# Kernel optimization log

Measured on AMD Instinct MI355X. Metric: run time of the kernel, lower is better.

## Reference

```python
import jax, jax.numpy as jnp
import numpy as np

N_NODES = 50000
D = 128
DROP_P = 0.2


def sage_conv(x, edge_index, W_l, W_r, b):
    # PyG SAGEConv (mean aggr): out = lin_l(mean_j x_j) + lin_r(x)
    src, dst = edge_index[0], edge_index[1]
    n = x.shape[0]
    agg = jax.ops.segment_sum(x[src], dst, num_segments=n)          # [N, F]
    cnt = jax.ops.segment_sum(jnp.ones((src.shape[0],), x.dtype), dst, num_segments=n)
    mean = agg / jnp.maximum(cnt, 1.0)[:, None]
    return mean @ W_l.T + x @ W_r.T + b


def setup_inputs() -> dict:
    key = jax.random.key(0)
    ks = jax.random.split(key, 9)
    x = jax.random.normal(ks[0], (N_NODES, D), dtype=jnp.float32)
    edge_index = jax.random.randint(ks[1], (2, 800000), 0, N_NODES, dtype=jnp.int64)
    s = 1.0 / np.sqrt(D)
    W1_l = jax.random.uniform(ks[2], (D, D), jnp.float32, -s, s)
    W1_r = jax.random.uniform(ks[3], (D, D), jnp.float32, -s, s)
    b1 = jax.random.uniform(ks[4], (D,), jnp.float32, -s, s)
    W2_l = jax.random.uniform(ks[5], (D, D), jnp.float32, -s, s)
    W2_r = jax.random.uniform(ks[6], (D, D), jnp.float32, -s, s)
    b2 = jax.random.uniform(ks[7], (D,), jnp.float32, -s, s)
    return {"x": x, "edge_index": edge_index, "W1_l": W1_l, "W1_r": W1_r,
            "b1": b1, "W2_l": W2_l, "W2_r": W2_r, "b2": b2}


def reference(x, edge_index, W1_l, W1_r, b1, W2_l, W2_r, b2):
    h = sage_conv(x, edge_index, W1_l, W1_r, b1)
    h = jax.nn.relu(h)
    # F.dropout(p=0.2) defaults to training=True; deterministic fixed-key mask
    keep = jax.random.bernoulli(jax.random.key(42), 1.0 - DROP_P, h.shape)
    h = jnp.where(keep, h / (1.0 - DROP_P), 0.0)
    return sage_conv(h, edge_index, W2_l, W2_r, b2)
```

## Files before the change

kernel.cpp:

```cpp
#include <hip/hip_runtime.h>
#include <stdint.h>

#define N_NODES 50000
#define D 128
#define N_EDGES 800000
#define NBUCK 196
#define BCAP 8192
#define EPB 4096

typedef __attribute__((ext_vector_type(8))) short bf16x8;
typedef __attribute__((ext_vector_type(4))) float f32x4;

__device__ __forceinline__ unsigned short f2bf(float f){
  unsigned u = __float_as_uint(f);
  u = u + 0x7FFFu + ((u >> 16) & 1u);
  return (unsigned short)(u >> 16);
}
__device__ __forceinline__ void acc2(float& a, float& b, unsigned w){
  a += __uint_as_float(w << 16);
  b += __uint_as_float(w & 0xFFFF0000u);
}

__device__ __forceinline__ unsigned rotl32(unsigned x, int r){
  return (x << r) | (x >> (32 - r));
}
__device__ __forceinline__ float dropout_factor(unsigned idx){
  unsigned x0 = 0u, x1 = idx;
  const unsigned ks0 = 0u;
  const unsigned ks1 = 42u;
  const unsigned ks2 = 0x1BD11BDAu ^ 0u ^ 42u;
  x0 += ks0; x1 += ks1;
  #define TFR(r) { x0 += x1; x1 = rotl32(x1,(r)); x1 ^= x0; }
  TFR(13) TFR(15) TFR(26) TFR(6)   x0 += ks1; x1 += ks2 + 1u;
  TFR(17) TFR(29) TFR(16) TFR(24)  x0 += ks2; x1 += ks0 + 2u;
  TFR(13) TFR(15) TFR(26) TFR(6)   x0 += ks0; x1 += ks1 + 3u;
  TFR(17) TFR(29) TFR(16) TFR(24)  x0 += ks1; x1 += ks2 + 4u;
  TFR(13) TFR(15) TFR(26) TFR(6)   x0 += ks2; x1 += ks0 + 5u;
  #undef TFR
  unsigned bits = x0 ^ x1;
  float u = __uint_as_float(0x3F800000u | (bits >> 9)) - 1.0f;
  return (u < 0.8f) ? 1.25f : 0.0f;
}

__global__ __launch_bounds__(256) void prep_kernel(
    const float* __restrict__ x,
    const float* __restrict__ W1l, const float* __restrict__ W1r,
    const float* __restrict__ W2l, const float* __restrict__ W2r,
    unsigned short* __restrict__ A1cat,
    unsigned short* __restrict__ Wcat1, unsigned short* __restrict__ Wcat2,
    int* __restrict__ gcursor, const void* __restrict__ ei, int* __restrict__ flag)
{
  int b = blockIdx.x, t = threadIdx.x;
  if (b < 6250){
    int i = b * 256 + t;
    int r = i >> 5, c4 = (i & 31) * 4;
    float4 v = *(const float4*)(x + (size_t)r * 128 + c4);
    ushort4 o = make_ushort4(f2bf(v.x), f2bf(v.y), f2bf(v.z), f2bf(v.w));
    *(ushort4*)(A1cat + (size_t)r * 256 + 128 + c4) = o;
  } else if (b < 6506){
    int c = (b < 6378) ? (b - 6250) : (b - 6378);
    const float* Wl = (b < 6378) ? W1l : W2l;
    const float* Wr = (b < 6378) ? W1r : W2r;
    unsigned short* Wc = (b < 6378) ? Wcat1 : Wcat2;
    float v = (t < 128) ? Wl[c * 128 + t] : Wr[c * 128 + (t - 128)];
    Wc[c * 256 + t] = f2bf(v);
  } else if (b == 6506){
    if (t < NBUCK) gcursor[t] = 0;
  } else {
    __shared__ int nz;
    if (t == 0) nz = 0;
    __syncthreads();
    const int* p = (const int*)ei;
    int local = 0;
    for (int i = t; i < 1024; i += 256)
      if (p[2 * i + 1] != 0) local = 1;
    if (local) atomicAdd(&nz, 1);
    __syncthreads();
    if (t == 0) *flag = (nz == 0) ? 1 : 0;
  }
}

__global__ __launch_bounds__(256) void bucket_kernel(const void* __restrict__ ei,
                                                     const int* __restrict__ flag,
                                                     int* __restrict__ gcursor,
                                                     int* __restrict__ buck){
  __shared__ int hist[NBUCK];
  __shared__ int baseoff[NBUCK];
  const int t = threadIdx.x;
  const int base = blockIdx.x * EPB;
  for (int i = t; i < NBUCK; i += 256) hist[i] = 0;
  __syncthreads();

  int pk[16], bk[16], rk[16];
  #pragma unroll
  for (int j = 0; j < 16; ++j) bk[j] = -1;

  if (*flag){
    const long long* p = (const long long*)ei;
    #pragma unroll
    for (int k = 0; k < 8; ++k){
      int e = base + (k * 256 + t) * 2;
      if (e < N_EDGES){
        int4 vs = *(const int4*)(p + e);
        int4 vd = *(const int4*)(p + N_EDGES + e);
        int ss0 = vs.x, ss1 = vs.z, dd0 = vd.x, dd1 = vd.z;
        int j0 = k * 2, j1 = k * 2 + 1;
        bk[j0] = dd0 >> 8; pk[j0] = (ss0 << 8) | (dd0 & 255);
        rk[j0] = atomicAdd(&hist[bk[j0]], 1);
        bk[j1] = dd1 >> 8; pk[j1] = (ss1 << 8) | (dd1 & 255);
        rk[j1] = atomicAdd(&hist[bk[j1]], 1);
      }
    }
  } else {
    const int* p = (const int*)ei;
    #pragma unroll
    for (int k = 0; k < 4; ++k){
      int e = base + (k * 256 + t) * 4;
      if (e < N_EDGES){
        int4 vs = *(const int4*)(p + e);
        int4 vd = *(const int4*)(p + N_EDGES + e);
        int ss[4] = {vs.x, vs.y, vs.z, vs.w};
        int dd[4] = {vd.x, vd.y, vd.z, vd.w};
        #pragma unroll
        for (int j = 0; j < 4; ++j){
          int slot = k * 4 + j;
          int d = dd[j];
          bk[slot] = d >> 8;
          pk[slot] = (ss[j] << 8) | (d & 255);
          rk[slot] = atomicAdd(&hist[bk[slot]], 1);
        }
      }
    }
  }
  __syncthreads();
  for (int i = t; i < NBUCK; i += 256){
    int h = hist[i];
    baseoff[i] = h ? atomicAdd(&gcursor[i], h) : 0;
  }
  __syncthreads();
  #pragma unroll
  for (int j = 0; j < 16; ++j){
    if (bk[j] >= 0)
      buck[bk[j] * BCAP + baseoff[bk[j]] + rk[j]] = pk[j];
  }
}

__global__ __launch_bounds__(256) void bscan_kernel(const int* __restrict__ gcursor,
                                                    int* __restrict__ bucket_base,
                                                    int* __restrict__ rowptr){
  __shared__ int s[256];
  int t = threadIdx.x;
  s[t] = (t < NBUCK) ? gcursor[t] : 0;
  __syncthreads();
  #pragma unroll
  for (int off = 1; off < 256; off <<= 1){
    int u = (t >= off) ? s[t - off] : 0;
    __syncthreads();
    s[t] += u;
    __syncthreads();
  }
  if (t < NBUCK) bucket_base[t] = (t == 0) ? 0 : s[t - 1];
  if (t == 0){ bucket_base[NBUCK] = N_EDGES; rowptr[N_NODES] = N_EDGES; }
}

__global__ __launch_bounds__(256) void csr_kernel(const int* __restrict__ gcursor,
                                                  const int* __restrict__ bucket_base,
                                                  const int* __restrict__ buck,
                                                  unsigned short* __restrict__ csr16,
                                                  int* __restrict__ rowptr){
  __shared__ int h[256];
  __shared__ int s[256];
  __shared__ int cur[256];
  const int b = blockIdx.x, t = threadIdx.x;
  const int cntb  = gcursor[b];
  const int gbase = bucket_base[b];
  h[t] = 0;
  __syncthreads();
  for (int i = t; i < cntb; i += 256)
    atomicAdd(&h[buck[b * BCAP + i] & 255], 1);
  __syncthreads();
  s[t] = h[t];
  __syncthreads();
  #pragma unroll
  for (int off = 1; off < 256; off <<= 1){
    int u = (t >= off) ? s[t - off] : 0;
    __syncthreads();
    s[t] += u;
    __syncthreads();
  }
  int excl = s[t] - h[t];
  int node = b * 256 + t;
  if (node < N_NODES) rowptr[node] = gbase + excl;
  cur[t] = gbase + excl;
  __syncthreads();
  for (int i = t; i < cntb; i += 256){
    int pkv = buck[b * BCAP + i];
    int pos = atomicAdd(&cur[pkv & 255], 1);
    csr16[pos] = (unsigned short)(((unsigned)pkv) >> 8);
  }
}

__global__ __launch_bounds__(256) void agg_bf16_kernel(
    unsigned short* __restrict__ Acat, const int* __restrict__ rowptr,
    const unsigned short* __restrict__ csr16)
{
  int node = blockIdx.x * 4 + (threadIdx.x >> 6);
  int lane = threadIdx.x & 63;
  if (node >= N_NODES) return;
  int q  = lane >> 4;
  int fl = lane & 15;
  int e0 = rowptr[node], e1 = rowptr[node + 1];
  float s0=0.f,s1=0.f,s2=0.f,s3=0.f,s4=0.f,s5=0.f,s6=0.f,s7=0.f;

  int e = e0;
  for (; e + 8 <= e1; e += 8){
    int ia = csr16[e + q];
    int ib = csr16[e + 4 + q];
    int4 va = *(const int4*)(Acat + (size_t)ia * 256 + 128 + fl * 8);
    int4 vb = *(const int4*)(Acat + (size_t)ib * 256 + 128 + fl * 8);
    acc2(s0, s1, (unsigned)va.x); acc2(s2, s3, (unsigned)va.y);
    acc2(s4, s5, (unsigned)va.z); acc2(s6, s7, (unsigned)va.w);
    acc2(s0, s1, (unsigned)vb.x); acc2(s2, s3, (unsigned)vb.y);
    acc2(s4, s5, (unsigned)vb.z); acc2(s6, s7, (unsigned)vb.w);
  }
  for (; e < e1; e += 4){
    int ee = e + q;
    if (ee < e1){
      int ia = csr16[ee];
      int4 va = *(const int4*)(Acat + (size_t)ia * 256 + 128 + fl * 8);
      acc2(s0, s1, (unsigned)va.x); acc2(s2, s3, (unsigned)va.y);
      acc2(s4, s5, (unsigned)va.z); acc2(s6, s7, (unsigned)va.w);
    }
  }
  s0 += __shfl_xor(s0, 16); s0 += __shfl_xor(s0, 32);
  s1 += __shfl_xor(s1, 16); s1 += __shfl_xor(s1, 32);
  s2 += __shfl_xor(s2, 16); s2 += __shfl_xor(s2, 32);
  s3 += __shfl_xor(s3, 16); s3 += __shfl_xor(s3, 32);
  s4 += __shfl_xor(s4, 16); s4 += __shfl_xor(s4, 32);
  s5 += __shfl_xor(s5, 16); s5 += __shfl_xor(s5, 32);
  s6 += __shfl_xor(s6, 16); s6 += __shfl_xor(s6, 32);
  s7 += __shfl_xor(s7, 16); s7 += __shfl_xor(s7, 32);
  if (q == 0){
    float inv = 1.0f / fmaxf((float)(e1 - e0), 1.0f);
    unsigned short ob[8] = { f2bf(s0*inv), f2bf(s1*inv), f2bf(s2*inv), f2bf(s3*inv),
                             f2bf(s4*inv), f2bf(s5*inv), f2bf(s6*inv), f2bf(s7*inv) };
    int4 o;
    o.x = (unsigned)ob[0] | ((unsigned)ob[1] << 16);
    o.y = (unsigned)ob[2] | ((unsigned)ob[3] << 16);
    o.z = (unsigned)ob[4] | ((unsigned)ob[5] << 16);
    o.w = (unsigned)ob[6] | ((unsigned)ob[7] << 16);
    *(int4*)(Acat + (size_t)node * 256 + fl * 8) = o;
  }
}

__global__ __launch_bounds__(256) void gemm_mfma(
    const unsigned short* __restrict__ Acat, const unsigned short* __restrict__ Wcat,
    const float* __restrict__ bias, void* __restrict__ outp, int mode)
{
  __shared__ __align__(16) char smem[64 * 132 * 4];
  const int t   = threadIdx.x;
  const int w   = t >> 6;
  const int tl  = t & 63;
  const int m15 = tl & 15;
  const int q   = tl >> 4;
  const int row0 = blockIdx.x * 64;

  bf16x8 bfr[2][8];
  #pragma unroll
  for (int ct = 0; ct < 2; ++ct){
    int col = w * 32 + ct * 16 + m15;
    #pragma unroll
    for (int kc = 0; kc < 8; ++kc)
      bfr[ct][kc] = *(const bf16x8*)(Wcat + (size_t)col * 256 + kc * 32 + q * 8);
  }

  #pragma unroll
  for (int u = 0; u < 8; ++u){
    int g   = t + 256 * u;
    int row = g >> 5, ch = g & 31;
    int kc  = ch >> 2, qq = ch & 3;
    int f   = (row >> 4) * 8 + kc;
    int slot = (row & 15) + 16 * qq;
    int gr = row0 + row; if (gr > N_NODES - 1) gr = N_NODES - 1;
    int4 v = *(const int4*)((const char*)Acat + (size_t)gr * 512 + ch * 16);
    *(int4*)(smem + (size_t)(f * 64 + (slot ^ kc)) * 16) = v;
  }
  __syncthreads();

  f32x4 acc[4][2];
  #pragma unroll
  for (int rt = 0; rt < 4; ++rt)
    #pragma unroll
    for (int ct = 0; ct < 2; ++ct)
      acc[rt][ct] = (f32x4){0.f, 0.f, 0.f, 0.f};

  #pragma unroll
  for (int kc = 0; kc < 8; ++kc){
    bf16x8 a[4];
    #pragma unroll
    for (int rt = 0; rt < 4; ++rt)
      a[rt] = *(const bf16x8*)(smem + (size_t)((rt * 8 + kc) * 64 + (tl ^ kc)) * 16);
    #pragma unroll
    for (int rt = 0; rt < 4; ++rt)
      #pragma unroll
      for (int ct = 0; ct < 2; ++ct)
        acc[rt][ct] = __builtin_amdgcn_mfma_f32_16x16x32_bf16(a[rt], bfr[ct][kc], acc[rt][ct], 0, 0, 0);
  }
  __syncthreads();

  float* sf = (float*)smem;
  #pragma unroll
  for (int rt = 0; rt < 4; ++rt)
    #pragma unroll
    for (int ct = 0; ct < 2; ++ct)
      #pragma unroll
      for (int i = 0; i < 4; ++i){
        int row = rt * 16 + q * 4 + i;
        int col = w * 32 + ct * 16 + m15;
        sf[row * 132 + col] = acc[rt][ct][i];
      }
  __syncthreads();

  if (mode == 1){
    unsigned short* hout = (unsigned short*)outp;
    #pragma unroll
    for (int v = 0; v < 4; ++v){
      int s = t + 256 * v;
      int row = s >> 4, c8 = (s & 15) * 8;
      int gr = row0 + row;
      if (gr < N_NODES){
        float4 p0 = *(const float4*)&sf[row * 132 + c8];
        float4 p1 = *(const float4*)&sf[row * 132 + c8 + 4];
        float vals[8] = {p0.x, p0.y, p0.z, p0.w, p1.x, p1.y, p1.z, p1.w};
        unsigned short ob[8];
        #pragma unroll
        for (int j = 0; j < 8; ++j){
          float vv = vals[j] + bias[c8 + j];
          vv = fmaxf(vv, 0.0f);
          vv *= dropout_factor((unsigned)(gr * 128 + c8 + j));
          ob[j] = f2bf(vv);
        }
        int4 o;
        o.x = (unsigned)ob[0] | ((unsigned)ob[1] << 16);
        o.y = (unsigned)ob[2] | ((unsigned)ob[3] << 16);
        o.z = (unsigned)ob[4] | ((unsigned)ob[5] << 16);
        o.w = (unsigned)ob[6] | ((unsigned)ob[7] << 16);
        *(int4*)(hout + (size_t)gr * 256 + 128 + c8) = o;
      }
    }
  } else {
    float* of = (float*)outp;
    #pragma unroll
    for (int v = 0; v < 8; ++v){
      int s = t + 256 * v;
      int row = s >> 5, c4 = (s & 31) * 4;
      int gr = row0 + row;
      if (gr < N_NODES){
        float4 p = *(const float4*)&sf[row * 132 + c4];
        p.x += bias[c4 + 0]; p.y += bias[c4 + 1];
        p.z += bias[c4 + 2]; p.w += bias[c4 + 3];
        *(float4*)(of + (size_t)gr * 128 + c4) = p;
      }
    }
  }
}

extern "C" void kernel_launch(void* const* d_in, const int* in_sizes, int n_in,
                              void* d_out, int out_size, void* d_ws, size_t ws_size,
                              hipStream_t stream)
{
  const float* x   = (const float*)d_in[0];
  const void*  ei  = d_in[1];
  const float* W1l = (const float*)d_in[2];
  const float* W1r = (const float*)d_in[3];
  const float* b1  = (const float*)d_in[4];
  const float* W2l = (const float*)d_in[5];
  const float* W2r = (const float*)d_in[6];
  const float* b2  = (const float*)d_in[7];

  char* ws = (char*)d_ws;
  unsigned short* A1cat = (unsigned short*)ws;
  size_t off = (size_t)N_NODES * 256 * sizeof(unsigned short);
  int* rowptr      = (int*)(ws + off);  off += (size_t)(N_NODES + 1) * sizeof(int);
  off = (off + 15) & ~(size_t)15;
  unsigned short* csr16 = (unsigned short*)(ws + off); off += (size_t)N_EDGES * sizeof(unsigned short);
  int* gcursor     = (int*)(ws + off);  off += NBUCK * sizeof(int);
  int* bucket_base = (int*)(ws + off);  off += (NBUCK + 1) * sizeof(int);
  int* flag        = (int*)(ws + off);  off += 16;
  off = (off + 15) & ~(size_t)15;
  int* buck        = (int*)(ws + off);  off += (size_t)NBUCK * BCAP * sizeof(int);
  unsigned short* Wcat1 = (unsigned short*)(ws + off); off += 128 * 256 * sizeof(unsigned short);
  unsigned short* Wcat2 = (unsigned short*)(ws + off); off += 128 * 256 * sizeof(unsigned short);

  unsigned short* A2cat = (unsigned short*)d_out;

  prep_kernel<<<6508, 256, 0, stream>>>(x, W1l, W1r, W2l, W2r, A1cat, Wcat1, Wcat2,
                                        gcursor, ei, flag);
  bucket_kernel<<<(N_EDGES + EPB - 1) / EPB, 256, 0, stream>>>(ei, flag, gcursor, buck);
  bscan_kernel<<<1, 256, 0, stream>>>(gcursor, bucket_base, rowptr);
  csr_kernel<<<NBUCK, 256, 0, stream>>>(gcursor, bucket_base, buck, csr16, rowptr);

  agg_bf16_kernel<<<(N_NODES + 3) / 4, 256, 0, stream>>>(A1cat, rowptr, csr16);
  gemm_mfma<<<(N_NODES + 63) / 64, 256, 0, stream>>>(A1cat, Wcat1, b1, (void*)A2cat, 1);
  agg_bf16_kernel<<<(N_NODES + 3) / 4, 256, 0, stream>>>(A2cat, rowptr, csr16);
  gemm_mfma<<<(N_NODES + 63) / 64, 256, 0, stream>>>(A2cat, Wcat2, b2, d_out, 0);

  (void)in_sizes; (void)n_in; (void)out_size; (void)ws_size;
}
```

Measured before the change: 216.9 us.

## Fuse neighbor aggregation into GEMM kernel and merge prep/bucket/scan launches

Aggregation is now done inside the MFMA GEMM kernel: each block gathers and averages neighbor rows straight into the LDS A-tile, so the mean no longer goes to global memory and back. The prep and bucket kernels are merged, the int64 check is redone per block, and the bucket scan moves into the CSR kernel, cutting the launch count from eight to four plus a memset. In exchange, the gather now uses one edge at a time per 16-lane group with less memory-level parallelism than the old 4-way split across the wave, and every CSR block redundantly rescans the bucket counts.

```diff
diff --git a/kernel.cpp b/kernel.cpp
--- a/kernel.cpp
+++ b/kernel.cpp
@@ -42,13 +42,13 @@
   return (u < 0.8f) ? 1.25f : 0.0f;
 }
 
-__global__ __launch_bounds__(256) void prep_kernel(
+__global__ __launch_bounds__(256) void prep_bucket_kernel(
     const float* __restrict__ x,
     const float* __restrict__ W1l, const float* __restrict__ W1r,
     const float* __restrict__ W2l, const float* __restrict__ W2r,
-    unsigned short* __restrict__ A1cat,
+    unsigned short* __restrict__ Xbf,
     unsigned short* __restrict__ Wcat1, unsigned short* __restrict__ Wcat2,
-    int* __restrict__ gcursor, const void* __restrict__ ei, int* __restrict__ flag)
+    const void* __restrict__ ei, int* __restrict__ gcursor, int* __restrict__ buck)
 {
   int b = blockIdx.x, t = threadIdx.x;
   if (b < 6250){
@@ -56,46 +56,41 @@
     int r = i >> 5, c4 = (i & 31) * 4;
     float4 v = *(const float4*)(x + (size_t)r * 128 + c4);
     ushort4 o = make_ushort4(f2bf(v.x), f2bf(v.y), f2bf(v.z), f2bf(v.w));
-    *(ushort4*)(A1cat + (size_t)r * 256 + 128 + c4) = o;
-  } else if (b < 6506){
+    *(ushort4*)(Xbf + (size_t)r * 128 + c4) = o;
+    return;
+  }
+  if (b < 6506){
     int c = (b < 6378) ? (b - 6250) : (b - 6378);
     const float* Wl = (b < 6378) ? W1l : W2l;
     const float* Wr = (b < 6378) ? W1r : W2r;
     unsigned short* Wc = (b < 6378) ? Wcat1 : Wcat2;
     float v = (t < 128) ? Wl[c * 128 + t] : Wr[c * 128 + (t - 128)];
     Wc[c * 256 + t] = f2bf(v);
-  } else if (b == 6506){
-    if (t < NBUCK) gcursor[t] = 0;
-  } else {
-    __shared__ int nz;
-    if (t == 0) nz = 0;
-    __syncthreads();
+    return;
+  }
+  __shared__ int hist[NBUCK];
+  __shared__ int baseoff[NBUCK];
+  __shared__ int nz;
+  const int bb = b - 6506;
+  const int base = bb * EPB;
+  if (t == 0) nz = 0;
+  for (int i = t; i < NBUCK; i += 256) hist[i] = 0;
+  __syncthreads();
+  {
     const int* p = (const int*)ei;
     int local = 0;
     for (int i = t; i < 1024; i += 256)
       if (p[2 * i + 1] != 0) local = 1;
     if (local) atomicAdd(&nz, 1);
-    __syncthreads();
-    if (t == 0) *flag = (nz == 0) ? 1 : 0;
-  }
-}
-
-__global__ __launch_bounds__(256) void bucket_kernel(const void* __restrict__ ei,
-                                                     const int* __restrict__ flag,
-                                                     int* __restrict__ gcursor,
-                                                     int* __restrict__ buck){
-  __shared__ int hist[NBUCK];
-  __shared__ int baseoff[NBUCK];
-  const int t = threadIdx.x;
-  const int base = blockIdx.x * EPB;
-  for (int i = t; i < NBUCK; i += 256) hist[i] = 0;
-  __syncthreads();
+  }
+  __syncthreads();
+  const int is64 = (nz == 0);
 
   int pk[16], bk[16], rk[16];
   #pragma unroll
   for (int j = 0; j < 16; ++j) bk[j] = -1;
 
-  if (*flag){
+  if (is64){
     const long long* p = (const long long*)ei;
     #pragma unroll
     for (int k = 0; k < 8; ++k){
@@ -103,11 +98,10 @@
       if (e < N_EDGES){
         int4 vs = *(const int4*)(p + e);
         int4 vd = *(const int4*)(p + N_EDGES + e);
-        int ss0 = vs.x, ss1 = vs.z, dd0 = vd.x, dd1 = vd.z;
         int j0 = k * 2, j1 = k * 2 + 1;
-        bk[j0] = dd0 >> 8; pk[j0] = (ss0 << 8) | (dd0 & 255);
+        bk[j0] = vd.x >> 8; pk[j0] = (vs.x << 8) | (vd.x & 255);
         rk[j0] = atomicAdd(&hist[bk[j0]], 1);
-        bk[j1] = dd1 >> 8; pk[j1] = (ss1 << 8) | (dd1 & 255);
+        bk[j1] = vd.z >> 8; pk[j1] = (vs.z << 8) | (vd.z & 255);
         rk[j1] = atomicAdd(&hist[bk[j1]], 1);
       }
     }
@@ -124,9 +118,8 @@
         #pragma unroll
         for (int j = 0; j < 4; ++j){
           int slot = k * 4 + j;
-          int d = dd[j];
-          bk[slot] = d >> 8;
-          pk[slot] = (ss[j] << 8) | (d & 255);
+          bk[slot] = dd[j] >> 8;
+          pk[slot] = (ss[j] << 8) | (dd[j] & 255);
           rk[slot] = atomicAdd(&hist[bk[slot]], 1);
         }
       }
@@ -145,12 +138,32 @@
   }
 }
 
-__global__ __launch_bounds__(256) void bscan_kernel(const int* __restrict__ gcursor,
-                                                    int* __restrict__ bucket_base,
-                                                    int* __restrict__ rowptr){
+__global__ __launch_bounds__(256) void csr_kernel(const int* __restrict__ gcursor,
+                                                  const int* __restrict__ buck,
+                                                  unsigned short* __restrict__ csr16,
+                                                  int* __restrict__ rowptr){
+  __shared__ int sb[256];
+  __shared__ int h[256];
   __shared__ int s[256];
-  int t = threadIdx.x;
-  s[t] = (t < NBUCK) ? gcursor[t] : 0;
+  __shared__ int cur[256];
+  const int b = blockIdx.x, t = threadIdx.x;
+  sb[t] = (t < NBUCK) ? gcursor[t] : 0;
+  __syncthreads();
+  #pragma unroll
+  for (int off = 1; off < 256; off <<= 1){
+    int u = (t >= off) ? sb[t - off] : 0;
+    __syncthreads();
+    sb[t] += u;
+    __syncthreads();
+  }
+  const int gbase = (b == 0) ? 0 : sb[b - 1];
+  const int cntb  = gcursor[b];
+  h[t] = 0;
+  __syncthreads();
+  for (int i = t; i < cntb; i += 256)
+    atomicAdd(&h[buck[b * BCAP + i] & 255], 1);
+  __syncthreads();
+  s[t] = h[t];
   __syncthreads();
   #pragma unroll
   for (int off = 1; off < 256; off <<= 1){
@@ -159,38 +172,10 @@
     s[t] += u;
     __syncthreads();
   }
-  if (t < NBUCK) bucket_base[t] = (t == 0) ? 0 : s[t - 1];
-  if (t == 0){ bucket_base[NBUCK] = N_EDGES; rowptr[N_NODES] = N_EDGES; }
-}
-
-__global__ __launch_bounds__(256) void csr_kernel(const int* __restrict__ gcursor,
-                                                  const int* __restrict__ bucket_base,
-                                                  const int* __restrict__ buck,
-                                                  unsigned short* __restrict__ csr16,
-                                                  int* __restrict__ rowptr){
-  __shared__ int h[256];
-  __shared__ int s[256];
-  __shared__ int cur[256];
-  const int b = blockIdx.x, t = threadIdx.x;
-  const int cntb  = gcursor[b];
-  const int gbase = bucket_base[b];
-  h[t] = 0;
-  __syncthreads();
-  for (int i = t; i < cntb; i += 256)
-    atomicAdd(&h[buck[b * BCAP + i] & 255], 1);
-  __syncthreads();
-  s[t] = h[t];
-  __syncthreads();
-  #pragma unroll
-  for (int off = 1; off < 256; off <<= 1){
-    int u = (t >= off) ? s[t - off] : 0;
-    __syncthreads();
-    s[t] += u;
-    __syncthreads();
-  }
   int excl = s[t] - h[t];
   int node = b * 256 + t;
   if (node < N_NODES) rowptr[node] = gbase + excl;
+  if (b == 0 && t == 0) rowptr[N_NODES] = N_EDGES;
   cur[t] = gbase + excl;
   __syncthreads();
   for (int i = t; i < cntb; i += 256){
@@ -200,62 +185,11 @@
   }
 }
 
-__global__ __launch_bounds__(256) void agg_bf16_kernel(
-    unsigned short* __restrict__ Acat, const int* __restrict__ rowptr,
-    const unsigned short* __restrict__ csr16)
-{
-  int node = blockIdx.x * 4 + (threadIdx.x >> 6);
-  int lane = threadIdx.x & 63;
-  if (node >= N_NODES) return;
-  int q  = lane >> 4;
-  int fl = lane & 15;
-  int e0 = rowptr[node], e1 = rowptr[node + 1];
-  float s0=0.f,s1=0.f,s2=0.f,s3=0.f,s4=0.f,s5=0.f,s6=0.f,s7=0.f;
-
-  int e = e0;
-  for (; e + 8 <= e1; e += 8){
-    int ia = csr16[e + q];
-    int ib = csr16[e + 4 + q];
-    int4 va = *(const int4*)(Acat + (size_t)ia * 256 + 128 + fl * 8);
-    int4 vb = *(const int4*)(Acat + (size_t)ib * 256 + 128 + fl * 8);
-    acc2(s0, s1, (unsigned)va.x); acc2(s2, s3, (unsigned)va.y);
-    acc2(s4, s5, (unsigned)va.z); acc2(s6, s7, (unsigned)va.w);
-    acc2(s0, s1, (unsigned)vb.x); acc2(s2, s3, (unsigned)vb.y);
-    acc2(s4, s5, (unsigned)vb.z); acc2(s6, s7, (unsigned)vb.w);
-  }
-  for (; e < e1; e += 4){
-    int ee = e + q;
-    if (ee < e1){
-      int ia = csr16[ee];
-      int4 va = *(const int4*)(Acat + (size_t)ia * 256 + 128 + fl * 8);
-      acc2(s0, s1, (unsigned)va.x); acc2(s2, s3, (unsigned)va.y);
-      acc2(s4, s5, (unsigned)va.z); acc2(s6, s7, (unsigned)va.w);
-    }
-  }
-  s0 += __shfl_xor(s0, 16); s0 += __shfl_xor(s0, 32);
-  s1 += __shfl_xor(s1, 16); s1 += __shfl_xor(s1, 32);
-  s2 += __shfl_xor(s2, 16); s2 += __shfl_xor(s2, 32);
-  s3 += __shfl_xor(s3, 16); s3 += __shfl_xor(s3, 32);
-  s4 += __shfl_xor(s4, 16); s4 += __shfl_xor(s4, 32);
-  s5 += __shfl_xor(s5, 16); s5 += __shfl_xor(s5, 32);
-  s6 += __shfl_xor(s6, 16); s6 += __shfl_xor(s6, 32);
-  s7 += __shfl_xor(s7, 16); s7 += __shfl_xor(s7, 32);
-  if (q == 0){
-    float inv = 1.0f / fmaxf((float)(e1 - e0), 1.0f);
-    unsigned short ob[8] = { f2bf(s0*inv), f2bf(s1*inv), f2bf(s2*inv), f2bf(s3*inv),
-                             f2bf(s4*inv), f2bf(s5*inv), f2bf(s6*inv), f2bf(s7*inv) };
-    int4 o;
-    o.x = (unsigned)ob[0] | ((unsigned)ob[1] << 16);
-    o.y = (unsigned)ob[2] | ((unsigned)ob[3] << 16);
-    o.z = (unsigned)ob[4] | ((unsigned)ob[5] << 16);
-    o.w = (unsigned)ob[6] | ((unsigned)ob[7] << 16);
-    *(int4*)(Acat + (size_t)node * 256 + fl * 8) = o;
-  }
-}
-
-__global__ __launch_bounds__(256) void gemm_mfma(
-    const unsigned short* __restrict__ Acat, const unsigned short* __restrict__ Wcat,
-    const float* __restrict__ bias, void* __restrict__ outp, int mode)
+__global__ __launch_bounds__(256) void fused_kernel(
+    const unsigned short* __restrict__ Xsrc,
+    const int* __restrict__ rowptr, const unsigned short* __restrict__ csr16,
+    const unsigned short* __restrict__ Wcat, const float* __restrict__ bias,
+    void* __restrict__ outp, int mode)
 {
   __shared__ __align__(16) char smem[64 * 132 * 4];
   const int t   = threadIdx.x;
@@ -275,15 +209,54 @@
   }
 
   #pragma unroll
-  for (int u = 0; u < 8; ++u){
+  for (int u = 0; u < 4; ++u){
     int g   = t + 256 * u;
-    int row = g >> 5, ch = g & 31;
-    int kc  = ch >> 2, qq = ch & 3;
-    int f   = (row >> 4) * 8 + kc;
+    int row = g >> 4, c = g & 15;
+    int gr = row0 + row; if (gr > N_NODES - 1) gr = N_NODES - 1;
+    int4 v = *(const int4*)(Xsrc + (size_t)gr * 128 + c * 8);
+    int kc = 4 + (c >> 2), qq = c & 3;
+    int f  = (row >> 4) * 8 + kc;
     int slot = (row & 15) + 16 * qq;
-    int gr = row0 + row; if (gr > N_NODES - 1) gr = N_NODES - 1;
-    int4 v = *(const int4*)((const char*)Acat + (size_t)gr * 512 + ch * 16);
     *(int4*)(smem + (size_t)(f * 64 + (slot ^ kc)) * 16) = v;
+  }
+
+  #pragma unroll
+  for (int i = 0; i < 4; ++i){
+    int row  = w * 16 + q * 4 + i;
+    int node = row0 + row;
+    float s0=0.f,s1=0.f,s2=0.f,s3=0.f,s4=0.f,s5=0.f,s6=0.f,s7=0.f;
+    float inv = 0.f;
+    if (node < N_NODES){
+      int e0 = rowptr[node], e1 = rowptr[node + 1];
+      int e = e0;
+      for (; e + 2 <= e1; e += 2){
+        int ia = csr16[e], ib = csr16[e + 1];
+        int4 va = *(const int4*)(Xsrc + (size_t)ia * 128 + m15 * 8);
+        int4 vb = *(const int4*)(Xsrc + (size_t)ib * 128 + m15 * 8);
+        acc2(s0, s1, (unsigned)va.x); acc2(s2, s3, (unsigned)va.y);
+        acc2(s4, s5, (unsigned)va.z); acc2(s6, s7, (unsigned)va.w);
+        acc2(s0, s1, (unsigned)vb.x); acc2(s2, s3, (unsigned)vb.y);
+        acc2(s4, s5, (unsigned)vb.z); acc2(s6, s7, (unsigned)vb.w);
+      }
+      if (e < e1){
+        int ia = csr16[e];
+        int4 va = *(const int4*)(Xsrc + (size_t)ia * 128 + m15 * 8);
+        acc2(s0, s1, (unsigned)va.x); acc2(s2, s3, (unsigned)va.y);
+        acc2(s4, s5, (unsigned)va.z); acc2(s6, s7, (unsigned)va.w);
+      }
+      inv = 1.0f / fmaxf((float)(e1 - e0), 1.0f);
+    }
+    unsigned short ob[8] = { f2bf(s0*inv), f2bf(s1*inv), f2bf(s2*inv), f2bf(s3*inv),
+                             f2bf(s4*inv), f2bf(s5*inv), f2bf(s6*inv), f2bf(s7*inv) };
+    int4 o;
+    o.x = (unsigned)ob[0] | ((unsigned)ob[1] << 16);
+    o.y = (unsigned)ob[2] | ((unsigned)ob[3] << 16);
+    o.z = (unsigned)ob[4] | ((unsigned)ob[5] << 16);
+    o.w = (unsigned)ob[6] | ((unsigned)ob[7] << 16);
+    int kc = m15 >> 2, qq = m15 & 3;
+    int f  = (row >> 4) * 8 + kc;
+    int slot = (row & 15) + 16 * qq;
+    *(int4*)(smem + (size_t)(f * 64 + (slot ^ kc)) * 16) = o;
   }
   __syncthreads();
 
@@ -345,7 +318,7 @@
         o.y = (unsigned)ob[2] | ((unsigned)ob[3] << 16);
         o.z = (unsigned)ob[4] | ((unsigned)ob[5] << 16);
         o.w = (unsigned)ob[6] | ((unsigned)ob[7] << 16);
-        *(int4*)(hout + (size_t)gr * 256 + 128 + c8) = o;
+        *(int4*)(hout + (size_t)gr * 128 + c8) = o;
       }
     }
   } else {
@@ -379,31 +352,27 @@
   const float* b2  = (const float*)d_in[7];
 
   char* ws = (char*)d_ws;
-  unsigned short* A1cat = (unsigned short*)ws;
-  size_t off = (size_t)N_NODES * 256 * sizeof(unsigned short);
+  size_t off = 0;
+  unsigned short* Xbf = (unsigned short*)(ws + off); off += (size_t)N_NODES * 128 * 2;
+  unsigned short* hbf = (unsigned short*)(ws + off); off += (size_t)N_NODES * 128 * 2;
   int* rowptr      = (int*)(ws + off);  off += (size_t)(N_NODES + 1) * sizeof(int);
   off = (off + 15) & ~(size_t)15;
-  unsigned short* csr16 = (unsigned short*)(ws + off); off += (size_t)N_EDGES * sizeof(unsigned short);
+  unsigned short* csr16 = (unsigned short*)(ws + off); off += (size_t)N_EDGES * 2;
   int* gcursor     = (int*)(ws + off);  off += NBUCK * sizeof(int);
-  int* bucket_base = (int*)(ws + off);  off += (NBUCK + 1) * sizeof(int);
-  int* flag        = (int*)(ws + off);  off += 16;
   off = (off + 15) & ~(size_t)15;
   int* buck        = (int*)(ws + off);  off += (size_t)NBUCK * BCAP * sizeof(int);
-  unsigned short* Wcat1 = (unsigned short*)(ws + off); off += 128 * 256 * sizeof(unsigned short);
-  unsigned short* Wcat2 = (unsigned short*)(ws + off); off += 128 * 256 * sizeof(unsigned short);
-
-  unsigned short* A2cat = (unsigned short*)d_out;
-
-  prep_kernel<<<6508, 256, 0, stream>>>(x, W1l, W1r, W2l, W2r, A1cat, Wcat1, Wcat2,
-                                        gcursor, ei, flag);
-  bucket_kernel<<<(N_EDGES + EPB - 1) / EPB, 256, 0, stream>>>(ei, flag, gcursor, buck);
-  bscan_kernel<<<1, 256, 0, stream>>>(gcursor, bucket_base, rowptr);
-  csr_kernel<<<NBUCK, 256, 0, stream>>>(gcursor, bucket_base, buck, csr16, rowptr);
-
-  agg_bf16_kernel<<<(N_NODES + 3) / 4, 256, 0, stream>>>(A1cat, rowptr, csr16);
-  gemm_mfma<<<(N_NODES + 63) / 64, 256, 0, stream>>>(A1cat, Wcat1, b1, (void*)A2cat, 1);
-  agg_bf16_kernel<<<(N_NODES + 3) / 4, 256, 0, stream>>>(A2cat, rowptr, csr16);
-  gemm_mfma<<<(N_NODES + 63) / 64, 256, 0, stream>>>(A2cat, Wcat2, b2, d_out, 0);
+  unsigned short* Wcat1 = (unsigned short*)(ws + off); off += 128 * 256 * 2;
+  unsigned short* Wcat2 = (unsigned short*)(ws + off); off += 128 * 256 * 2;
+
+  hipMemsetAsync(gcursor, 0, NBUCK * sizeof(int), stream);
+  prep_bucket_kernel<<<6702, 256, 0, stream>>>(x, W1l, W1r, W2l, W2r, Xbf,
+                                               Wcat1, Wcat2, ei, gcursor, buck);
+  csr_kernel<<<NBUCK, 256, 0, stream>>>(gcursor, buck, csr16, rowptr);
+
+  fused_kernel<<<(N_NODES + 63) / 64, 256, 0, stream>>>(Xbf, rowptr, csr16,
+                                                        Wcat1, b1, (void*)hbf, 1);
+  fused_kernel<<<(N_NODES + 63) / 64, 256, 0, stream>>>(hbf, rowptr, csr16,
+                                                        Wcat2, b2, d_out, 0);
 
   (void)in_sizes; (void)n_in; (void)out_size; (void)ws_size;
 }
```

New measurement: 286.3 us. 32.0% more time.

## Fuse prep with bucketing, fold bucket scan into CSR kernel, unroll gather

Applied to the files above, without the earlier changes.

Merges the conversion/prep kernel and the edge bucketing kernel into one launch. Each bucketing block now detects the index width itself, and the cursor reset moves to a memset. The single-block bucket prefix scan is dropped; every CSR block recomputes the 196-entry scan redundantly. The aggregation gather loop is unrolled to 16 edges per iteration to keep more loads in flight. This cuts two kernel launches and their serialization, at the cost of redundant scan work and more registers in the gather.

```diff
diff --git a/kernel.cpp b/kernel.cpp
--- a/kernel.cpp
+++ b/kernel.cpp
@@ -42,13 +42,13 @@
   return (u < 0.8f) ? 1.25f : 0.0f;
 }
 
-__global__ __launch_bounds__(256) void prep_kernel(
+__global__ __launch_bounds__(256) void prep_bucket_kernel(
     const float* __restrict__ x,
     const float* __restrict__ W1l, const float* __restrict__ W1r,
     const float* __restrict__ W2l, const float* __restrict__ W2r,
     unsigned short* __restrict__ A1cat,
     unsigned short* __restrict__ Wcat1, unsigned short* __restrict__ Wcat2,
-    int* __restrict__ gcursor, const void* __restrict__ ei, int* __restrict__ flag)
+    const void* __restrict__ ei, int* __restrict__ gcursor, int* __restrict__ buck)
 {
   int b = blockIdx.x, t = threadIdx.x;
   if (b < 6250){
@@ -57,45 +57,40 @@
     float4 v = *(const float4*)(x + (size_t)r * 128 + c4);
     ushort4 o = make_ushort4(f2bf(v.x), f2bf(v.y), f2bf(v.z), f2bf(v.w));
     *(ushort4*)(A1cat + (size_t)r * 256 + 128 + c4) = o;
-  } else if (b < 6506){
+    return;
+  }
+  if (b < 6506){
     int c = (b < 6378) ? (b - 6250) : (b - 6378);
     const float* Wl = (b < 6378) ? W1l : W2l;
     const float* Wr = (b < 6378) ? W1r : W2r;
     unsigned short* Wc = (b < 6378) ? Wcat1 : Wcat2;
     float v = (t < 128) ? Wl[c * 128 + t] : Wr[c * 128 + (t - 128)];
     Wc[c * 256 + t] = f2bf(v);
-  } else if (b == 6506){
-    if (t < NBUCK) gcursor[t] = 0;
-  } else {
-    __shared__ int nz;
-    if (t == 0) nz = 0;
-    __syncthreads();
+    return;
+  }
+  __shared__ int hist[NBUCK];
+  __shared__ int baseoff[NBUCK];
+  __shared__ int nz;
+  const int bb = b - 6506;
+  const int base = bb * EPB;
+  if (t == 0) nz = 0;
+  for (int i = t; i < NBUCK; i += 256) hist[i] = 0;
+  __syncthreads();
+  {
     const int* p = (const int*)ei;
     int local = 0;
     for (int i = t; i < 1024; i += 256)
       if (p[2 * i + 1] != 0) local = 1;
     if (local) atomicAdd(&nz, 1);
-    __syncthreads();
-    if (t == 0) *flag = (nz == 0) ? 1 : 0;
-  }
-}
-
-__global__ __launch_bounds__(256) void bucket_kernel(const void* __restrict__ ei,
-                                                     const int* __restrict__ flag,
-                                                     int* __restrict__ gcursor,
-                                                     int* __restrict__ buck){
-  __shared__ int hist[NBUCK];
-  __shared__ int baseoff[NBUCK];
-  const int t = threadIdx.x;
-  const int base = blockIdx.x * EPB;
-  for (int i = t; i < NBUCK; i += 256) hist[i] = 0;
-  __syncthreads();
+  }
+  __syncthreads();
+  const int is64 = (nz == 0);
 
   int pk[16], bk[16], rk[16];
   #pragma unroll
   for (int j = 0; j < 16; ++j) bk[j] = -1;
 
-  if (*flag){
+  if (is64){
     const long long* p = (const long long*)ei;
     #pragma unroll
     for (int k = 0; k < 8; ++k){
@@ -103,11 +98,10 @@
       if (e < N_EDGES){
         int4 vs = *(const int4*)(p + e);
         int4 vd = *(const int4*)(p + N_EDGES + e);
-        int ss0 = vs.x, ss1 = vs.z, dd0 = vd.x, dd1 = vd.z;
         int j0 = k * 2, j1 = k * 2 + 1;
-        bk[j0] = dd0 >> 8; pk[j0] = (ss0 << 8) | (dd0 & 255);
+        bk[j0] = vd.x >> 8; pk[j0] = (vs.x << 8) | (vd.x & 255);
         rk[j0] = atomicAdd(&hist[bk[j0]], 1);
-        bk[j1] = dd1 >> 8; pk[j1] = (ss1 << 8) | (dd1 & 255);
+        bk[j1] = vd.z >> 8; pk[j1] = (vs.z << 8) | (vd.z & 255);
         rk[j1] = atomicAdd(&hist[bk[j1]], 1);
       }
     }
@@ -124,9 +118,8 @@
         #pragma unroll
         for (int j = 0; j < 4; ++j){
           int slot = k * 4 + j;
-          int d = dd[j];
-          bk[slot] = d >> 8;
-          pk[slot] = (ss[j] << 8) | (d & 255);
+          bk[slot] = dd[j] >> 8;
+          pk[slot] = (ss[j] << 8) | (dd[j] & 255);
           rk[slot] = atomicAdd(&hist[bk[slot]], 1);
         }
       }
@@ -145,12 +138,32 @@
   }
 }
 
-__global__ __launch_bounds__(256) void bscan_kernel(const int* __restrict__ gcursor,
-                                                    int* __restrict__ bucket_base,
-                                                    int* __restrict__ rowptr){
+__global__ __launch_bounds__(256) void csr_kernel(const int* __restrict__ gcursor,
+                                                  const int* __restrict__ buck,
+                                                  unsigned short* __restrict__ csr16,
+                                                  int* __restrict__ rowptr){
+  __shared__ int sb[256];
+  __shared__ int h[256];
   __shared__ int s[256];
-  int t = threadIdx.x;
-  s[t] = (t < NBUCK) ? gcursor[t] : 0;
+  __shared__ int cur[256];
+  const int b = blockIdx.x, t = threadIdx.x;
+  sb[t] = (t < NBUCK) ? gcursor[t] : 0;
+  __syncthreads();
+  #pragma unroll
+  for (int off = 1; off < 256; off <<= 1){
+    int u = (t >= off) ? sb[t - off] : 0;
+    __syncthreads();
+    sb[t] += u;
+    __syncthreads();
+  }
+  const int gbase = (b == 0) ? 0 : sb[b - 1];
+  const int cntb  = gcursor[b];
+  h[t] = 0;
+  __syncthreads();
+  for (int i = t; i < cntb; i += 256)
+    atomicAdd(&h[buck[b * BCAP + i] & 255], 1);
+  __syncthreads();
+  s[t] = h[t];
   __syncthreads();
   #pragma unroll
   for (int off = 1; off < 256; off <<= 1){
@@ -159,38 +172,10 @@
     s[t] += u;
     __syncthreads();
   }
-  if (t < NBUCK) bucket_base[t] = (t == 0) ? 0 : s[t - 1];
-  if (t == 0){ bucket_base[NBUCK] = N_EDGES; rowptr[N_NODES] = N_EDGES; }
-}
-
-__global__ __launch_bounds__(256) void csr_kernel(const int* __restrict__ gcursor,
-                                                  const int* __restrict__ bucket_base,
-                                                  const int* __restrict__ buck,
-                                                  unsigned short* __restrict__ csr16,
-                                                  int* __restrict__ rowptr){
-  __shared__ int h[256];
-  __shared__ int s[256];
-  __shared__ int cur[256];
-  const int b = blockIdx.x, t = threadIdx.x;
-  const int cntb  = gcursor[b];
-  const int gbase = bucket_base[b];
-  h[t] = 0;
-  __syncthreads();
-  for (int i = t; i < cntb; i += 256)
-    atomicAdd(&h[buck[b * BCAP + i] & 255], 1);
-  __syncthreads();
-  s[t] = h[t];
-  __syncthreads();
-  #pragma unroll
-  for (int off = 1; off < 256; off <<= 1){
-    int u = (t >= off) ? s[t - off] : 0;
-    __syncthreads();
-    s[t] += u;
-    __syncthreads();
-  }
   int excl = s[t] - h[t];
   int node = b * 256 + t;
   if (node < N_NODES) rowptr[node] = gbase + excl;
+  if (b == 0 && t == 0) rowptr[N_NODES] = N_EDGES;
   cur[t] = gbase + excl;
   __syncthreads();
   for (int i = t; i < cntb; i += 256){
@@ -213,23 +198,41 @@
   float s0=0.f,s1=0.f,s2=0.f,s3=0.f,s4=0.f,s5=0.f,s6=0.f,s7=0.f;
 
   int e = e0;
+  for (; e + 16 <= e1; e += 16){
+    int i0 = csr16[e + q];
+    int i1 = csr16[e + 4 + q];
+    int i2 = csr16[e + 8 + q];
+    int i3 = csr16[e + 12 + q];
+    int4 v0 = *(const int4*)(Acat + (size_t)i0 * 256 + 128 + fl * 8);
+    int4 v1 = *(const int4*)(Acat + (size_t)i1 * 256 + 128 + fl * 8);
+    int4 v2 = *(const int4*)(Acat + (size_t)i2 * 256 + 128 + fl * 8);
+    int4 v3 = *(const int4*)(Acat + (size_t)i3 * 256 + 128 + fl * 8);
+    acc2(s0, s1, (unsigned)v0.x); acc2(s2, s3, (unsigned)v0.y);
+    acc2(s4, s5, (unsigned)v0.z); acc2(s6, s7, (unsigned)v0.w);
+    acc2(s0, s1, (unsigned)v1.x); acc2(s2, s3, (unsigned)v1.y);
+    acc2(s4, s5, (unsigned)v1.z); acc2(s6, s7, (unsigned)v1.w);
+    acc2(s0, s1, (unsigned)v2.x); acc2(s2, s3, (unsigned)v2.y);
+    acc2(s4, s5, (unsigned)v2.z); acc2(s6, s7, (unsigned)v2.w);
+    acc2(s0, s1, (unsigned)v3.x); acc2(s2, s3, (unsigned)v3.y);
+    acc2(s4, s5, (unsigned)v3.z); acc2(s6, s7, (unsigned)v3.w);
+  }
   for (; e + 8 <= e1; e += 8){
-    int ia = csr16[e + q];
-    int ib = csr16[e + 4 + q];
-    int4 va = *(const int4*)(Acat + (size_t)ia * 256 + 128 + fl * 8);
-    int4 vb = *(const int4*)(Acat + (size_t)ib * 256 + 128 + fl * 8);
-    acc2(s0, s1, (unsigned)va.x); acc2(s2, s3, (unsigned)va.y);
-    acc2(s4, s5, (unsigned)va.z); acc2(s6, s7, (unsigned)va.w);
-    acc2(s0, s1, (unsigned)vb.x); acc2(s2, s3, (unsigned)vb.y);
-    acc2(s4, s5, (unsigned)vb.z); acc2(s6, s7, (unsigned)vb.w);
+    int i0 = csr16[e + q];
+    int i1 = csr16[e + 4 + q];
+    int4 v0 = *(const int4*)(Acat + (size_t)i0 * 256 + 128 + fl * 8);
+    int4 v1 = *(const int4*)(Acat + (size_t)i1 * 256 + 128 + fl * 8);
+    acc2(s0, s1, (unsigned)v0.x); acc2(s2, s3, (unsigned)v0.y);
+    acc2(s4, s5, (unsigned)v0.z); acc2(s6, s7, (unsigned)v0.w);
+    acc2(s0, s1, (unsigned)v1.x); acc2(s2, s3, (unsigned)v1.y);
+    acc2(s4, s5, (unsigned)v1.z); acc2(s6, s7, (unsigned)v1.w);
   }
   for (; e < e1; e += 4){
     int ee = e + q;
     if (ee < e1){
-      int ia = csr16[ee];
-      int4 va = *(const int4*)(Acat + (size_t)ia * 256 + 128 + fl * 8);
-      acc2(s0, s1, (unsigned)va.x); acc2(s2, s3, (unsigned)va.y);
-      acc2(s4, s5, (unsigned)va.z); acc2(s6, s7, (unsigned)va.w);
+      int i0 = csr16[ee];
+      int4 v0 = *(const int4*)(Acat + (size_t)i0 * 256 + 128 + fl * 8);
+      acc2(s0, s1, (unsigned)v0.x); acc2(s2, s3, (unsigned)v0.y);
+      acc2(s4, s5, (unsigned)v0.z); acc2(s6, s7, (unsigned)v0.w);
     }
   }
   s0 += __shfl_xor(s0, 16); s0 += __shfl_xor(s0, 32);
@@ -385,8 +388,6 @@
   off = (off + 15) & ~(size_t)15;
   unsigned short* csr16 = (unsigned short*)(ws + off); off += (size_t)N_EDGES * sizeof(unsigned short);
   int* gcursor     = (int*)(ws + off);  off += NBUCK * sizeof(int);
-  int* bucket_base = (int*)(ws + off);  off += (NBUCK + 1) * sizeof(int);
-  int* flag        = (int*)(ws + off);  off += 16;
   off = (off + 15) & ~(size_t)15;
   int* buck        = (int*)(ws + off);  off += (size_t)NBUCK * BCAP * sizeof(int);
   unsigned short* Wcat1 = (unsigned short*)(ws + off); off += 128 * 256 * sizeof(unsigned short);
@@ -394,11 +395,10 @@
 
   unsigned short* A2cat = (unsigned short*)d_out;
 
-  prep_kernel<<<6508, 256, 0, stream>>>(x, W1l, W1r, W2l, W2r, A1cat, Wcat1, Wcat2,
-                                        gcursor, ei, flag);
-  bucket_kernel<<<(N_EDGES + EPB - 1) / EPB, 256, 0, stream>>>(ei, flag, gcursor, buck);
-  bscan_kernel<<<1, 256, 0, stream>>>(gcursor, bucket_base, rowptr);
-  csr_kernel<<<NBUCK, 256, 0, stream>>>(gcursor, bucket_base, buck, csr16, rowptr);
+  hipMemsetAsync(gcursor, 0, NBUCK * sizeof(int), stream);
+  prep_bucket_kernel<<<6702, 256, 0, stream>>>(x, W1l, W1r, W2l, W2r, A1cat,
+                                               Wcat1, Wcat2, ei, gcursor, buck);
+  csr_kernel<<<NBUCK, 256, 0, stream>>>(gcursor, buck, csr16, rowptr);
 
   agg_bf16_kernel<<<(N_NODES + 3) / 4, 256, 0, stream>>>(A1cat, rowptr, csr16);
   gemm_mfma<<<(N_NODES + 63) / 64, 256, 0, stream>>>(A1cat, Wcat1, b1, (void*)A2cat, 1);
```

New measurement: 218.6 us. Within noise of the previous version (+0.8%).
